# Kernel optimization log

Measured on AMD Instinct MI355X. Metric: run time of the kernel, lower is better.

Reference implementation:

```python
import jax, jax.numpy as jnp
import numpy as np

EPS = 1e-06
K = 32


def setup_inputs() -> dict:
    key = jax.random.key(0)
    k1, k2, k3, k4, k5 = jax.random.split(key, 5)
    d_model, n_latents = 1024, 16384
    x = jax.random.normal(k1, (2, 2048, d_model), dtype=jnp.float32)
    b_pre = jax.random.normal(k2, (d_model,), dtype=jnp.float32) * 0.02
    W_enc = jax.random.normal(k3, (n_latents, d_model), dtype=jnp.float32) / np.sqrt(d_model)
    b_enc = jax.random.normal(k4, (n_latents,), dtype=jnp.float32) * 0.02
    W_dec = jax.random.normal(k5, (d_model, n_latents), dtype=jnp.float32)
    # mimic normalize_decoder_weights: unit norm along dim=1 (n_latents axis per row)
    W_dec = W_dec / jnp.linalg.norm(W_dec, axis=1, keepdims=True)
    return {"x": x, "b_pre": b_pre, "W_enc": W_enc, "b_enc": b_enc, "W_dec": W_dec}


def reference(x, b_pre, W_enc, b_enc, W_dec):
    B, S, D = x.shape
    # preprocess: center + normalize (torch .std is unbiased, ddof=1)
    mean = jnp.mean(x, axis=-1, keepdims=True)
    norm = jnp.std(x, axis=-1, keepdims=True, ddof=1) + EPS
    xn = ((x - mean) / norm).reshape(-1, D)          # [N, D]
    # encode
    h = (xn - b_pre) @ W_enc.T + b_enc               # [N, n_latents]
    # top-k + relu + scatter into sparse latent
    vals, idx = jax.lax.top_k(h, K)                  # [N, K]
    vals = jax.nn.relu(vals)
    rows = jnp.arange(h.shape[0])[:, None]
    h_sparse = jnp.zeros_like(h).at[rows, idx].set(vals)
    # decode (dense matmul over mostly-zero latents, as in the original)
    recon = h_sparse @ W_dec.T + b_pre               # [N, D]
    # postprocess: denormalize
    recon = recon.reshape(B, S, D) * norm + mean
    return recon
```

## Files before the change

kernel.cpp:

```cpp
#include <hip/hip_runtime.h>
#include <cstdint>
#include <cstddef>

typedef _Float16 half_t;
typedef _Float16 half4_t __attribute__((ext_vector_type(4)));
typedef _Float16 half8_t __attribute__((ext_vector_type(8)));
typedef unsigned short ushort8_t __attribute__((ext_vector_type(8)));
typedef float floatx4 __attribute__((ext_vector_type(4)));

#define NROWS 4096
#define DMODEL 1024
#define NLAT 16384
#define CAND_MAX 256

#define MBYTE (1ull << 20)
static const size_t oW0    = 0;
static const size_t oWdT   = 32 * MBYTE;
static const size_t oMeanF = 64 * MBYTE;
static const size_t oNormF = 64 * MBYTE + (64ull << 10);
static const size_t oMeanD = 64 * MBYTE + (128ull << 10);
static const size_t oNormD = 64 * MBYTE + (192ull << 10);
static const size_t oCandC = 64 * MBYTE + (256ull << 10);
static const size_t oCandI = 65 * MBYTE;
static const size_t oCandV = 69 * MBYTE;
static const size_t oBatch = 77 * MBYTE;

#define BATCH_ROW_BYTES 34816ull

__device__ __forceinline__ void gload16(const void* g, void* l) {
  __builtin_amdgcn_global_load_lds(
      (const __attribute__((address_space(1))) void*)g,
      (__attribute__((address_space(3))) void*)l, 16, 0, 0);
}

__device__ __forceinline__ uint32_t okey16(uint32_t u) {
  return (u & 0x8000u) ? ((~u) & 0xFFFFu) : (u | 0x8000u);
}
__device__ __forceinline__ float inv_okey16(uint32_t k) {
  unsigned short u = (k & 0x8000u) ? (unsigned short)(k & 0x7FFFu)
                                   : (unsigned short)(~k);
  return (float)__builtin_bit_cast(_Float16, u);
}

#define WSPLIT_B 2048
#define TRANS_B  4096
__global__ __launch_bounds__(256) void prepro_kernel(
    const float* __restrict__ x, const float* __restrict__ b_pre,
    const float* __restrict__ W_enc, const float* __restrict__ Wd,
    half_t* __restrict__ W0h, half_t* __restrict__ WdT,
    half_t* __restrict__ X0,
    float* __restrict__ meanF, float* __restrict__ normF,
    double* __restrict__ meanD, double* __restrict__ normD, int r0) {
  int bid = blockIdx.x, tid = threadIdx.x;
  if (bid < WSPLIT_B) {
    size_t base = (size_t)bid * 2048 + tid;
    for (int it = 0; it < 8; ++it) {
      size_t i = base + (size_t)it * 256;
      float4 v = ((const float4*)W_enc)[i];
      half4_t h0;
      h0[0] = (half_t)(v.x * 1024.0f);
      h0[1] = (half_t)(v.y * 1024.0f);
      h0[2] = (half_t)(v.z * 1024.0f);
      h0[3] = (half_t)(v.w * 1024.0f);
      ((half4_t*)W0h)[i] = h0;
    }
    return;
  }
  if (bid < WSPLIT_B + TRANS_B) {
    __shared__ float tile[64][65];
    int t = bid - WSPLIT_B;
    int c0 = (t & 255) * 64;
    int r0t = (t >> 8) * 64;
    int tc = tid & 63, tg = tid >> 6;
    for (int i = 0; i < 16; ++i) {
      int rr = i * 4 + tg;
      tile[rr][tc] = Wd[(size_t)(r0t + rr) * NLAT + c0 + tc];
    }
    __syncthreads();
    for (int i = 0; i < 16; ++i) {
      int cc = i * 4 + tg;
      WdT[(size_t)(c0 + cc) * DMODEL + r0t + tc] = (half_t)tile[tc][cc];
    }
    return;
  }
  int rl = bid - WSPLIT_B - TRANS_B;
  int rg = r0 + rl;
  const float4* px = (const float4*)(x + (size_t)rg * DMODEL);
  float4 v = px[tid];
  double s  = (double)v.x + (double)v.y + (double)v.z + (double)v.w;
  double sq = (double)v.x * v.x + (double)v.y * v.y +
              (double)v.z * v.z + (double)v.w * v.w;
  for (int off = 32; off; off >>= 1) {
    s += __shfl_down(s, off);
    sq += __shfl_down(sq, off);
  }
  __shared__ double ss[4], ssq[4];
  __shared__ double sMean, sNorm;
  int wv = tid >> 6, ln = tid & 63;
  if (ln == 0) { ss[wv] = s; ssq[wv] = sq; }
  __syncthreads();
  if (tid == 0) {
    double S = ss[0] + ss[1] + ss[2] + ss[3];
    double Q = ssq[0] + ssq[1] + ssq[2] + ssq[3];
    double mean = S / (double)DMODEL;
    double var = (Q - (double)DMODEL * mean * mean) / (double)(DMODEL - 1);
    double nrm = sqrt(var) + 1e-6;
    sMean = mean; sNorm = nrm;
    meanF[rg] = (float)mean; normF[rg] = (float)nrm;
    meanD[rg] = mean;        normD[rg] = nrm;
  }
  __syncthreads();
  float mean = (float)sMean, nrm = (float)sNorm;
  const float4* pb = (const float4*)b_pre;
  float4 bp = pb[tid];
  float c[4];
  c[0] = ((v.x - mean) / nrm - bp.x) * 1024.0f;
  c[1] = ((v.y - mean) / nrm - bp.y) * 1024.0f;
  c[2] = ((v.z - mean) / nrm - bp.z) * 1024.0f;
  c[3] = ((v.w - mean) / nrm - bp.w) * 1024.0f;
  half4_t h0;
  for (int i = 0; i < 4; ++i) h0[i] = (half_t)c[i];
  ((half4_t*)(X0 + (size_t)rl * DMODEL))[tid] = h0;
}

__global__ __launch_bounds__(256, 4) void gemm_enc(
    const half_t* __restrict__ X0, const half_t* __restrict__ W0,
    const float* __restrict__ b_enc, half_t* __restrict__ h) {
  __shared__ __align__(16) half_t As[128 * 64];
  __shared__ __align__(16) half_t Bs[128 * 64];
  int tid = threadIdx.x;
  int lane = tid & 63, w = tid >> 6;
  int lin = blockIdx.y * gridDim.x + blockIdx.x;
  int xcd = lin & 7;
  int q = lin >> 3;
  int bn = xcd * 16 + (q & 15);
  int bm = q >> 4;
  int wr = w >> 1, wc = w & 1;
  floatx4 acc[4][4] = {};

  int ldrow = lane >> 3;
  int ldcol = (lane & 7) * 8;

  for (int kt = 0; kt < 16; ++kt) {
    int kph = kt * 64;
#pragma unroll
    for (int i = 0; i < 4; ++i) {
      int chunk = i * 4 + w;
      int row = chunk * 8 + ldrow;
      gload16(X0 + (size_t)(bm * 128 + row) * DMODEL + kph + ldcol,
              As + chunk * 512);
      gload16(W0 + (size_t)(bn * 128 + row) * DMODEL + kph + ldcol,
              Bs + chunk * 512);
    }
    __syncthreads();
#pragma unroll
    for (int kk = 0; kk < 2; ++kk) {
      half8_t a[4], b[4];
#pragma unroll
      for (int mi = 0; mi < 4; ++mi)
        a[mi] = *(const half8_t*)(As + (wr * 64 + mi * 16 + (lane & 15)) * 64 +
                                  kk * 32 + (lane >> 4) * 8);
#pragma unroll
      for (int ni = 0; ni < 4; ++ni)
        b[ni] = *(const half8_t*)(Bs + (wc * 64 + ni * 16 + (lane & 15)) * 64 +
                                  kk * 32 + (lane >> 4) * 8);
#pragma unroll
      for (int mi = 0; mi < 4; ++mi)
#pragma unroll
        for (int ni = 0; ni < 4; ++ni)
          acc[mi][ni] = __builtin_amdgcn_mfma_f32_16x16x32_f16(
              a[mi], b[ni], acc[mi][ni], 0, 0, 0);
    }
    __syncthreads();
  }

  const float scale = 0x1p-20f;
  int rbase = bm * 128 + wr * 64 + (lane >> 4) * 4;
  int cbase = bn * 128 + wc * 64 + (lane & 15);
#pragma unroll
  for (int mi = 0; mi < 4; ++mi)
#pragma unroll
    for (int ni = 0; ni < 4; ++ni) {
      int col = cbase + ni * 16;
      float be = b_enc[col];
#pragma unroll
      for (int r = 0; r < 4; ++r) {
        int row = rbase + mi * 16 + r;
        h[(size_t)row * NLAT + col] = (half_t)(acc[mi][ni][r] * scale + be);
      }
    }
}

__global__ __launch_bounds__(256) void cand_kernel(
    const half_t* __restrict__ h, int* __restrict__ candIdx,
    int* __restrict__ candCnt, int r0) {
  int rl = blockIdx.x, tid = threadIdx.x;
  int rg = r0 + rl;
  const ushort8_t* ph8 = (const ushort8_t*)(h + (size_t)rl * NLAT);
  __shared__ uint32_t hist[8192];
  __shared__ int chunkSum[256];
  __shared__ float sThresh;
  __shared__ int cCount;

  for (int i = tid; i < 8192; i += 256) hist[i] = 0;
  if (tid == 0) cCount = 0;
  __syncthreads();

  for (int i = 0; i < 8; ++i) {
    ushort8_t v = ph8[tid + i * 256];
#pragma unroll
    for (int e = 0; e < 8; ++e)
      atomicAdd(&hist[okey16((uint32_t)v[e]) >> 3], 1u);
  }
  __syncthreads();
  {
    int s = 0;
    for (int b = 0; b < 32; ++b) s += (int)hist[tid * 32 + b];
    chunkSum[tid] = s;
  }
  __syncthreads();
  if (tid == 0) {
    int cum = 0, cchunk = 255;
    for (; cchunk > 0; --cchunk) {
      if (cum + chunkSum[cchunk] >= 32) break;
      cum += chunkSum[cchunk];
    }
    int b = cchunk * 32 + 31;
    for (; b > 0; --b) {
      if (cum + (int)hist[b] >= 32) break;
      cum += (int)hist[b];
    }
    sThresh = inv_okey16((uint32_t)b << 3) - 0.02f;
  }
  __syncthreads();
  float thresh = sThresh;

  for (int i = 0; i < 8; ++i) {
    ushort8_t v = ph8[tid + i * 256];
#pragma unroll
    for (int e = 0; e < 8; ++e) {
      float f = (float)__builtin_bit_cast(_Float16, (unsigned short)v[e]);
      if (f >= thresh) {
        int j = (tid + i * 256) * 8 + e;
        int slot = atomicAdd(&cCount, 1);
        if (slot < CAND_MAX) candIdx[(size_t)rg * CAND_MAX + slot] = j;
      }
    }
  }
  __syncthreads();
  if (tid == 0) candCnt[rg] = (cCount < CAND_MAX) ? cCount : CAND_MAX;
}

__global__ __launch_bounds__(256) void refine_dot(
    const float* __restrict__ x, const float* __restrict__ b_pre,
    const float* __restrict__ W_enc, const float* __restrict__ b_enc,
    const double* __restrict__ meanD, const double* __restrict__ normD,
    const int* __restrict__ candIdx, const int* __restrict__ candCnt,
    double* __restrict__ candV, int r0) {
  int rg = r0 + blockIdx.x;
  int tid = threadIdx.x;
  int wv = tid >> 6, ln = tid & 63;
  double mean = meanD[rg], nrm = normD[rg];
  const float* px = x + (size_t)rg * DMODEL;
  double xr[16];
#pragma unroll
  for (int u = 0; u < 16; ++u)
    xr[u] = ((double)px[ln + u * 64] - mean) / nrm - (double)b_pre[ln + u * 64];
  int nc = candCnt[rg];
  const int* ci = candIdx + (size_t)rg * CAND_MAX;

  for (int c0 = wv * 4; c0 < nc; c0 += 16) {
    const float* wp[4];
#pragma unroll
    for (int q = 0; q < 4; ++q) {
      int c = c0 + q;
      int j = ci[c < nc ? c : (nc - 1)];
      wp[q] = W_enc + (size_t)j * DMODEL + ln;
    }
    double a0 = 0.0, a1 = 0.0, a2 = 0.0, a3 = 0.0;
#pragma unroll
    for (int u = 0; u < 16; ++u) {
      float w0 = wp[0][u * 64];
      float w1 = wp[1][u * 64];
      float w2 = wp[2][u * 64];
      float w3 = wp[3][u * 64];
      a0 += xr[u] * (double)w0;
      a1 += xr[u] * (double)w1;
      a2 += xr[u] * (double)w2;
      a3 += xr[u] * (double)w3;
    }
    double accq[4] = {a0, a1, a2, a3};
#pragma unroll
    for (int q = 0; q < 4; ++q) {
      double s = accq[q];
      for (int off = 32; off; off >>= 1) s += __shfl_down(s, off);
      int c = c0 + q;
      if (ln == 0 && c < nc) {
        int j = ci[c];
        candV[(size_t)rg * CAND_MAX + c] = s + (double)b_enc[j];
      }
    }
  }
}

__global__ __launch_bounds__(256) void sel_decode(
    const double* __restrict__ candV, const int* __restrict__ candIdx,
    const int* __restrict__ candCnt,
    const half_t* __restrict__ WdT, const float* __restrict__ b_pre,
    const float* __restrict__ meanF, const float* __restrict__ normF,
    float* __restrict__ out, int r0) {
  int rg = r0 + blockIdx.x, tid = threadIdx.x;
  __shared__ double cV[CAND_MAX];
  __shared__ int cI[CAND_MAX];
  __shared__ float sVal[32];
  __shared__ int sIdx[32];
  int nc = candCnt[rg];
  for (int c = tid; c < nc; c += 256) {
    cV[c] = candV[(size_t)rg * CAND_MAX + c];
    cI[c] = candIdx[(size_t)rg * CAND_MAX + c];
  }
  if (tid < 32) { sVal[tid] = 0.0f; sIdx[tid] = 0; }
  __syncthreads();
  for (int c = tid; c < nc; c += 256) {
    double v = cV[c];
    int ix = cI[c];
    int rank = 0;
    for (int o = 0; o < nc; ++o) {
      double vo = cV[o];
      int io = cI[o];
      rank += (vo > v || (vo == v && io < ix)) ? 1 : 0;
    }
    if (rank < 32) {
      sIdx[rank] = ix;
      sVal[rank] = (float)(v > 0.0 ? v : 0.0);
    }
  }
  __syncthreads();
  int d0 = tid * 4;
  float4 accv = {0.f, 0.f, 0.f, 0.f};
#pragma unroll 8
  for (int k = 0; k < 32; ++k) {
    float vk = sVal[k];
    const half4_t wv = *(const half4_t*)(WdT + (size_t)sIdx[k] * DMODEL + d0);
    accv.x += vk * (float)wv[0]; accv.y += vk * (float)wv[1];
    accv.z += vk * (float)wv[2]; accv.w += vk * (float)wv[3];
  }
  float4 bp = ((const float4*)b_pre)[tid];
  float nrm = normF[rg], mn = meanF[rg];
  float4 o;
  o.x = (accv.x + bp.x) * nrm + mn;
  o.y = (accv.y + bp.y) * nrm + mn;
  o.z = (accv.z + bp.z) * nrm + mn;
  o.w = (accv.w + bp.w) * nrm + mn;
  ((float4*)(out + (size_t)rg * DMODEL))[tid] = o;
}

extern "C" void kernel_launch(void* const* d_in, const int* in_sizes, int n_in,
                              void* d_out, int out_size, void* d_ws, size_t ws_size,
                              hipStream_t stream) {
  const float* x     = (const float*)d_in[0];
  const float* b_pre = (const float*)d_in[1];
  const float* W_enc = (const float*)d_in[2];
  const float* b_enc = (const float*)d_in[3];
  const float* W_dec = (const float*)d_in[4];
  float* out = (float*)d_out;
  char* ws = (char*)d_ws;

  int rowsB = NROWS;
  while (rowsB > 128) {
    size_t need = oBatch + (size_t)rowsB * BATCH_ROW_BYTES;
    if (need <= ws_size) break;
    rowsB >>= 1;
  }
  if (oBatch + (size_t)rowsB * BATCH_ROW_BYTES > ws_size) return;

  half_t* W0 = (half_t*)(ws + oW0);
  half_t* WdT = (half_t*)(ws + oWdT);
  float* meanF = (float*)(ws + oMeanF);
  float* normF = (float*)(ws + oNormF);
  double* meanD = (double*)(ws + oMeanD);
  double* normD = (double*)(ws + oNormD);
  int*   candCnt = (int*)(ws + oCandC);
  int*   candIdx = (int*)(ws + oCandI);
  double* candV  = (double*)(ws + oCandV);
  half_t* X0b  = (half_t*)(ws + oBatch);
  half_t* hb   = X0b + (size_t)rowsB * DMODEL;

  for (int r0 = 0; r0 < NROWS; r0 += rowsB) {
    hipLaunchKernelGGL(prepro_kernel,
                       dim3(WSPLIT_B + TRANS_B + rowsB), dim3(256), 0, stream,
                       x, b_pre, W_enc, W_dec, W0, WdT, X0b,
                       meanF, normF, meanD, normD, r0);
    hipLaunchKernelGGL(gemm_enc, dim3(NLAT / 128, rowsB / 128), dim3(256), 0, stream,
                       X0b, W0, b_enc, hb);
    hipLaunchKernelGGL(cand_kernel, dim3(rowsB), dim3(256), 0, stream,
                       hb, candIdx, candCnt, r0);
    hipLaunchKernelGGL(refine_dot, dim3(rowsB), dim3(256), 0, stream,
                       x, b_pre, W_enc, b_enc, meanD, normD, candIdx, candCnt,
                       candV, r0);
    hipLaunchKernelGGL(sel_decode, dim3(rowsB), dim3(256), 0, stream,
                       candV, candIdx, candCnt, WdT, b_pre, meanF, normF, out, r0);
  }
}
```

Baseline: 383.3 us.

## Rewrite encoder GEMM with 256x256 tiles, double-buffered LDS, and XOR swizzle

The encoder GEMM moves from 128x128 tiles with 4 waves and single-buffered LDS to 256x256 tiles with 8 waves, double-buffered LDS staging, and an XOR swizzle on LDS addresses. Loads for k-tile kt+2 are issued while tile kt is being computed, using vmcnt waits and raw barriers, and s_setprio raises priority around the MFMA block. The aim is to hide global load latency, avoid LDS bank conflicts and raise arithmetic intensity. In exchange it uses 128KB of LDS and more accumulators per block, which lowers occupancy and requires batch rows in multiples of 256.

```diff
diff --git a/kernel.cpp b/kernel.cpp
--- a/kernel.cpp
+++ b/kernel.cpp
@@ -123,72 +123,102 @@
   ((half4_t*)(X0 + (size_t)rl * DMODEL))[tid] = h0;
 }
 
-__global__ __launch_bounds__(256, 4) void gemm_enc(
+__global__ __launch_bounds__(512, 2) void gemm_enc(
     const half_t* __restrict__ X0, const half_t* __restrict__ W0,
-    const float* __restrict__ b_enc, half_t* __restrict__ h) {
-  __shared__ __align__(16) half_t As[128 * 64];
-  __shared__ __align__(16) half_t Bs[128 * 64];
+    const float* __restrict__ b_enc, half_t* __restrict__ h, int mtiles) {
+  __shared__ __align__(16) half_t As[2][256 * 64];
+  __shared__ __align__(16) half_t Bs[2][256 * 64];
   int tid = threadIdx.x;
-  int lane = tid & 63, w = tid >> 6;
-  int lin = blockIdx.y * gridDim.x + blockIdx.x;
-  int xcd = lin & 7;
-  int q = lin >> 3;
-  int bn = xcd * 16 + (q & 15);
-  int bm = q >> 4;
-  int wr = w >> 1, wc = w & 1;
-  floatx4 acc[4][4] = {};
-
-  int ldrow = lane >> 3;
-  int ldcol = (lane & 7) * 8;
+  int lane = tid & 63, wave = tid >> 6;
+  int wm = wave >> 2, wn = wave & 3;
+
+  int bid = blockIdx.x;
+  int xcd = bid & 7, q = bid >> 3;
+  int bn = xcd * 8 + (q & 7);
+  int bm = q >> 3;
+  (void)mtiles;
+
+  const char* Ag = (const char*)(X0 + (size_t)bm * 256 * DMODEL);
+  const char* Bg = (const char*)(W0 + (size_t)bn * 256 * DMODEL);
+
+  int srcSwz = ((lane & 7) ^ (lane >> 3)) << 4;
+  int rowBase = wave * 8 + (lane >> 3);
+  int ldsWOff = wave * 1024;
+
+#define STAGE(b, kt)                                                          \
+  {                                                                           \
+    int colB = (kt) * 128 + srcSwz;                                           \
+    _Pragma("unroll") for (int i = 0; i < 4; ++i) {                           \
+      size_t go = (size_t)(i * 64 + rowBase) * 2048 + colB;                   \
+      gload16(Ag + go, (char*)As[b] + i * 8192 + ldsWOff);                    \
+      gload16(Bg + go, (char*)Bs[b] + i * 8192 + ldsWOff);                    \
+    }                                                                         \
+  }
+
+  floatx4 acc[8][4] = {};
+
+  STAGE(0, 0);
+  STAGE(1, 1);
+  asm volatile("s_waitcnt vmcnt(8)" ::: "memory");
+  __builtin_amdgcn_sched_barrier(0);
+  __builtin_amdgcn_s_barrier();
+  __builtin_amdgcn_sched_barrier(0);
+
+  int laneQ = (lane & 15) * 128 + (lane >> 4) * 16;
+  int sxor = (lane & 7) << 4;
+  int aRow = wm * 128 * 128;
+  int bRow = wn * 64 * 128;
 
   for (int kt = 0; kt < 16; ++kt) {
-    int kph = kt * 64;
-#pragma unroll
-    for (int i = 0; i < 4; ++i) {
-      int chunk = i * 4 + w;
-      int row = chunk * 8 + ldrow;
-      gload16(X0 + (size_t)(bm * 128 + row) * DMODEL + kph + ldcol,
-              As + chunk * 512);
-      gload16(W0 + (size_t)(bn * 128 + row) * DMODEL + kph + ldcol,
-              Bs + chunk * 512);
-    }
-    __syncthreads();
-#pragma unroll
+    int cur = kt & 1;
+    const char* Ab = (const char*)As[cur];
+    const char* Bb = (const char*)Bs[cur];
     for (int kk = 0; kk < 2; ++kk) {
-      half8_t a[4], b[4];
-#pragma unroll
-      for (int mi = 0; mi < 4; ++mi)
-        a[mi] = *(const half8_t*)(As + (wr * 64 + mi * 16 + (lane & 15)) * 64 +
-                                  kk * 32 + (lane >> 4) * 8);
+      int kOff = kk * 64 + laneQ;
+      half8_t a[8], b[4];
+#pragma unroll
+      for (int mi = 0; mi < 8; ++mi)
+        a[mi] = *(const half8_t*)(Ab + ((aRow + mi * 2048 + kOff) ^ sxor));
 #pragma unroll
       for (int ni = 0; ni < 4; ++ni)
-        b[ni] = *(const half8_t*)(Bs + (wc * 64 + ni * 16 + (lane & 15)) * 64 +
-                                  kk * 32 + (lane >> 4) * 8);
-#pragma unroll
-      for (int mi = 0; mi < 4; ++mi)
+        b[ni] = *(const half8_t*)(Bb + ((bRow + ni * 2048 + kOff) ^ sxor));
+      __builtin_amdgcn_s_setprio(1);
+#pragma unroll
+      for (int mi = 0; mi < 8; ++mi)
 #pragma unroll
         for (int ni = 0; ni < 4; ++ni)
           acc[mi][ni] = __builtin_amdgcn_mfma_f32_16x16x32_f16(
               a[mi], b[ni], acc[mi][ni], 0, 0, 0);
-    }
-    __syncthreads();
-  }
+      __builtin_amdgcn_s_setprio(0);
+    }
+    if (kt == 15) break;
+    __builtin_amdgcn_s_barrier();
+    if (kt + 2 < 16) {
+      STAGE(cur, kt + 2);
+      asm volatile("s_waitcnt vmcnt(8)" ::: "memory");
+    } else {
+      asm volatile("s_waitcnt vmcnt(0)" ::: "memory");
+    }
+    __builtin_amdgcn_sched_barrier(0);
+    __builtin_amdgcn_s_barrier();
+    __builtin_amdgcn_sched_barrier(0);
+  }
+#undef STAGE
 
   const float scale = 0x1p-20f;
-  int rbase = bm * 128 + wr * 64 + (lane >> 4) * 4;
-  int cbase = bn * 128 + wc * 64 + (lane & 15);
-#pragma unroll
-  for (int mi = 0; mi < 4; ++mi)
-#pragma unroll
-    for (int ni = 0; ni < 4; ++ni) {
-      int col = cbase + ni * 16;
-      float be = b_enc[col];
-#pragma unroll
-      for (int r = 0; r < 4; ++r) {
-        int row = rbase + mi * 16 + r;
-        h[(size_t)row * NLAT + col] = (half_t)(acc[mi][ni][r] * scale + be);
-      }
-    }
+  int rowb = bm * 256 + wm * 128 + ((lane >> 4) * 4);
+  int colb = bn * 256 + wn * 64 + (lane & 15);
+  float be[4];
+#pragma unroll
+  for (int ni = 0; ni < 4; ++ni) be[ni] = b_enc[colb + ni * 16];
+#pragma unroll
+  for (int mi = 0; mi < 8; ++mi)
+#pragma unroll
+    for (int ni = 0; ni < 4; ++ni)
+#pragma unroll
+      for (int r = 0; r < 4; ++r)
+        h[(size_t)(rowb + mi * 16 + r) * NLAT + colb + ni * 16] =
+            (half_t)(acc[mi][ni][r] * scale + be[ni]);
 }
 
 __global__ __launch_bounds__(256) void cand_kernel(
@@ -367,7 +397,7 @@
   char* ws = (char*)d_ws;
 
   int rowsB = NROWS;
-  while (rowsB > 128) {
+  while (rowsB > 256) {
     size_t need = oBatch + (size_t)rowsB * BATCH_ROW_BYTES;
     if (need <= ws_size) break;
     rowsB >>= 1;
@@ -391,8 +421,9 @@
                        dim3(WSPLIT_B + TRANS_B + rowsB), dim3(256), 0, stream,
                        x, b_pre, W_enc, W_dec, W0, WdT, X0b,
                        meanF, normF, meanD, normD, r0);
-    hipLaunchKernelGGL(gemm_enc, dim3(NLAT / 128, rowsB / 128), dim3(256), 0, stream,
-                       X0b, W0, b_enc, hb);
+    int mtiles = rowsB / 256;
+    hipLaunchKernelGGL(gemm_enc, dim3(mtiles * 64), dim3(512), 0, stream,
+                       X0b, W0, b_enc, hb, mtiles);
     hipLaunchKernelGGL(cand_kernel, dim3(rowsB), dim3(256), 0, stream,
                        hb, candIdx, candCnt, r0);
     hipLaunchKernelGGL(refine_dot, dim3(rowsB), dim3(256), 0, stream,
```

Result: no change. 378.2 us (-1.3%).
